# Kernel tuning notes

Measured on AMD Instinct MI355X. Metric: run time of the kernel, lower is better.

## Reference

```python
import jax, jax.numpy as jnp
import numpy as np

TEMPERATURE = 0.3
BASE_TEMPERATURE = 0.07
EPS = 1e-08


def setup_inputs() -> dict:
    key = jax.random.key(0)
    k1, k2 = jax.random.split(key)
    bsz, n_views, f_dim = 4096, 2, 128
    features = jax.random.normal(k1, (bsz, n_views, f_dim), dtype=jnp.float32)
    # L2-normalize as is standard for contrastive features (keeps logits well-scaled)
    features = features / jnp.linalg.norm(features, axis=-1, keepdims=True)
    labels = jax.random.randint(k2, (bsz,), 0, 2, dtype=jnp.int64)
    return {"features": features, "labels": labels}


def reference(features, labels):
    # features: [B, V, D], labels: [B]
    B, V, D = features.shape
    N = B * V

    # mask[i,j] = 1 if labels[i] == labels[j]
    mask = (labels[:, None] == labels[None, :]).astype(jnp.float32)  # [B, B]

    # torch.cat(torch.unbind(features, dim=1), dim=0): view-major stacking -> [V*B, D]
    contrast_feature = features.transpose(1, 0, 2).reshape(N, D)
    anchor_feature = contrast_feature  # contrast_mode == 'all'

    logits = jnp.matmul(anchor_feature, contrast_feature.T) / TEMPERATURE  # [N, N]
    logits = logits - jax.lax.stop_gradient(jnp.max(logits, axis=1, keepdims=True))

    mask = jnp.tile(mask, (V, V))  # [N, N]
    logits_mask = 1.0 - jnp.eye(N, dtype=jnp.float32)  # mask out self-contrast
    mask = mask * logits_mask

    exp_logits = jnp.exp(logits) * logits_mask
    log_prob = logits - jnp.log(jnp.sum(exp_logits, axis=1, keepdims=True) + EPS)

    mean_log_prob_pos = jnp.sum(mask * log_prob, axis=1) / (jnp.sum(mask, axis=1) + EPS)
    loss = -(TEMPERATURE / BASE_TEMPERATURE) * mean_log_prob_pos  # [N]
    return jnp.mean(loss.reshape(V, B))
```

## Files before the change

kernel.cpp:

```cpp
#include <hip/hip_runtime.h>
#include <hip/hip_bf16.h>

constexpr int B_SZ  = 4096;
constexpr int N_SZ  = 8192;
constexpr int CHUNK = 512;
constexpr int TILE  = 64;
constexpr int NT    = CHUNK / TILE;
constexpr int NCH   = N_SZ / CHUNK;
constexpr int BROWS = 128;

typedef __attribute__((ext_vector_type(8))) __bf16 bf16x8;
typedef __attribute__((ext_vector_type(4))) float f32x4;

#define SQRT_CSC  2.1929404f
#define SELF_EXP  28.0316248f
#define NEG_RATIO (-(0.3f / 0.07f))

__device__ __forceinline__ unsigned short f2bf(float f) {
    unsigned u = __float_as_uint(f);
    u += 0x7FFFu + ((u >> 16) & 1u);
    return (unsigned short)(u >> 16);
}

__device__ __forceinline__ void gl_lds16(const unsigned short* g, unsigned short* l) {
    __builtin_amdgcn_global_load_lds(
        (const __attribute__((address_space(1))) unsigned int*)g,
        (__attribute__((address_space(3))) unsigned int*)l, 16, 0, 0);
}

__global__ __launch_bounds__(256) void prep_kernel(const float* __restrict__ feat,
                                                   unsigned short* __restrict__ A,
                                                   float* __restrict__ out) {
    const int tid = threadIdx.x;
    if (blockIdx.x == 0 && tid == 0) out[0] = 0.f;
    int t = blockIdx.x * 256 + tid;
    int n = t >> 5;
    int q = (t & 31) << 2;
    int b = n & (B_SZ - 1);
    int v = n >> 12;
    const float4 f = *reinterpret_cast<const float4*>(feat + (((size_t)b * 2 + v) << 7) + q);
    ushort4 o;
    o.x = f2bf(f.x * SQRT_CSC); o.y = f2bf(f.y * SQRT_CSC);
    o.z = f2bf(f.z * SQRT_CSC); o.w = f2bf(f.w * SQRT_CSC);
    *reinterpret_cast<ushort4*>(A + (((size_t)n) << 7) + q) = o;
}

__global__ __launch_bounds__(256) void msum_kernel(const float* __restrict__ feat,
                                                   const int* __restrict__ labels,
                                                   float* __restrict__ mpart) {
    __shared__ float sm[2][256];
    const int tid = threadIdx.x;
    const int v = tid >> 7, d = tid & 127;
    const int b0 = blockIdx.x * 16;
    float a0 = 0.f, a1 = 0.f;
#pragma unroll
    for (int it = 0; it < 16; ++it) {
        const int b = b0 + it;
        const float x = feat[(((size_t)b * 2 + v) << 7) + d];
        if (labels[b]) a1 += x; else a0 += x;
    }
    sm[0][tid] = a0; sm[1][tid] = a1;
    __syncthreads();
    if (tid < 128)
        mpart[(size_t)tid * 256 + blockIdx.x] = sm[0][tid] + sm[0][tid + 128];
    else
        mpart[(size_t)tid * 256 + blockIdx.x] = sm[1][tid - 128] + sm[1][tid];
}

__global__ __launch_bounds__(256) void mreduce_kernel(const float* __restrict__ mpart,
                                                      const int* __restrict__ labels,
                                                      float* __restrict__ mvec,
                                                      int* __restrict__ cnt) {
    __shared__ int redi[4];
    const int tid = threadIdx.x;
    const float* p = mpart + (size_t)tid * 256;
    float s = 0.f;
#pragma unroll 8
    for (int k = 0; k < 256; k += 4) {
        const float4 x = *reinterpret_cast<const float4*>(p + k);
        s += x.x + x.y + x.z + x.w;
    }
    mvec[tid] = s;
    int c = 0;
    for (int i = tid; i < B_SZ; i += 256) c += labels[i];
#pragma unroll
    for (int m = 1; m < 64; m <<= 1) c += __shfl_xor(c, m);
    if ((tid & 63) == 0) redi[tid >> 6] = c;
    __syncthreads();
    if (tid == 0) *cnt = redi[0] + redi[1] + redi[2] + redi[3];
}

__global__ __launch_bounds__(256, 2) void gram_kernel(const unsigned short* __restrict__ A,
                                                      float* __restrict__ S_part) {
    __shared__ __align__(16) unsigned short tb[2][TILE * 128];

    const int tid  = threadIdx.x;
    const int wave = tid >> 6;
    const int lane = tid & 63;
    const int grp  = lane >> 4;
    const int lc   = lane & 15;
    const int row0 = blockIdx.x * BROWS + wave * 32;
    const int col0 = blockIdx.y * CHUNK;

    bf16x8 a[2][4];
#pragma unroll
    for (int rt = 0; rt < 2; ++rt) {
        const unsigned short* ap = A + ((size_t)(row0 + 16 * rt + lc) << 7) + grp * 8;
#pragma unroll
        for (int g = 0; g < 4; ++g)
            a[rt][g] = *reinterpret_cast<const bf16x8*>(ap + g * 32);
    }

    int off[4];
#pragma unroll
    for (int g = 0; g < 4; ++g)
        off[g] = lc * 128 + (((4 * g + grp) ^ (lc & 7)) << 3);

    float s_acc[2][4] = {{0,0,0,0},{0,0,0,0}};

    auto stage = [&](int buf, int tt) {
        const unsigned short* gbase = A + ((size_t)(col0 + tt * TILE) << 7);
#pragma unroll
        for (int k = 0; k < 4; ++k) {
            const int s = tid + 256 * k;
            const int r = s >> 4, c = s & 15;
            const int src = (r << 4) + (c ^ (r & 7));
            gl_lds16(gbase + src * 8, &tb[buf][s * 8]);
        }
    };

    stage(0, 0);
    __syncthreads();

#pragma clang loop unroll(disable)
    for (int t = 0; t < NT; ++t) {
        const int cur = t & 1;
        if (t + 1 < NT) stage(cur ^ 1, t + 1);

        const unsigned short* bp = &tb[cur][0];
#pragma unroll
        for (int ct = 0; ct < 4; ++ct) {
            bf16x8 bfr[4];
#pragma unroll
            for (int g = 0; g < 4; ++g)
                bfr[g] = *reinterpret_cast<const bf16x8*>(bp + ct * 2048 + off[g]);

            f32x4 acc0 = {0,0,0,0}, acc1 = {0,0,0,0};
#pragma unroll
            for (int g = 0; g < 4; ++g) {
                acc0 = __builtin_amdgcn_mfma_f32_16x16x32_bf16(a[0][g], bfr[g], acc0, 0, 0, 0);
                acc1 = __builtin_amdgcn_mfma_f32_16x16x32_bf16(a[1][g], bfr[g], acc1, 0, 0, 0);
            }
#pragma unroll
            for (int r = 0; r < 4; ++r) {
                s_acc[0][r] += __builtin_amdgcn_exp2f(acc0[r]);
                s_acc[1][r] += __builtin_amdgcn_exp2f(acc1[r]);
            }
        }
        __syncthreads();
    }

#pragma unroll
    for (int m = 1; m < 16; m <<= 1)
#pragma unroll
        for (int rt = 0; rt < 2; ++rt)
#pragma unroll
            for (int r = 0; r < 4; ++r)
                s_acc[rt][r] += __shfl_xor(s_acc[rt][r], m);

    if (lc == 0) {
        const size_t base = (size_t)blockIdx.y * N_SZ;
#pragma unroll
        for (int rt = 0; rt < 2; ++rt)
#pragma unroll
            for (int r = 0; r < 4; ++r)
                S_part[base + row0 + 16 * rt + 4 * grp + r] = s_acc[rt][r];
    }
}

__global__ __launch_bounds__(256) void final_kernel(const float* __restrict__ S_part,
                                                    const float* __restrict__ feat,
                                                    const int* __restrict__ labels,
                                                    const float* __restrict__ mvec,
                                                    const int* __restrict__ cnt,
                                                    float* __restrict__ out) {
    __shared__ float red[4];
    const int tid = threadIdx.x;
    const int i = blockIdx.x * 256 + tid;

    float S = -SELF_EXP;
#pragma unroll
    for (int k = 0; k < NCH; ++k) S += S_part[(size_t)k * N_SZ + i];

    const int b = i & (B_SZ - 1), v = i >> 12;
    const int lab = labels[b];
    const float* fr = feat + (((size_t)b * 2 + v) << 7);
    const float* mv = mvec + (lab ? 128 : 0);
    float dot = 0.f;
#pragma unroll 8
    for (int d = 0; d < 128; d += 4) {
        const float4 x = *reinterpret_cast<const float4*>(fr + d);
        const float4 y = *reinterpret_cast<const float4*>(mv + d);
        dot += x.x * y.x + x.y * y.y + x.z * y.z + x.w * y.w;
    }

    const int c1 = *cnt;
    const int cs = lab ? c1 : (B_SZ - c1);
    const float n = (float)(2 * cs - 1);
    float term = ((dot - 1.0f) * (1.0f / 0.3f) - n * logf(S + 1e-8f)) / (n + 1e-8f);

#pragma unroll
    for (int m = 1; m < 64; m <<= 1) term += __shfl_xor(term, m);
    if ((tid & 63) == 0) red[tid >> 6] = term;
    __syncthreads();
    if (tid == 0)
        atomicAdd(out, (red[0] + red[1] + red[2] + red[3]) * (NEG_RATIO / (float)N_SZ));
}

extern "C" void kernel_launch(void* const* d_in, const int* in_sizes, int n_in,
                              void* d_out, int out_size, void* d_ws, size_t ws_size,
                              hipStream_t stream) {
    const float* feat = (const float*)d_in[0];
    const int* labels = (const int*)d_in[1];
    float* out = (float*)d_out;

    char* ws = (char*)d_ws;
    unsigned short* A = (unsigned short*)ws;
    float* S_part = (float*)(ws + (size_t)2 * 1024 * 1024);
    float* mpart  = (float*)(ws + (size_t)2 * 1024 * 1024 + 512 * 1024);
    float* mvec   = (float*)(ws + (size_t)2 * 1024 * 1024 + 768 * 1024);
    int*   cnt    = (int*)(ws + (size_t)2 * 1024 * 1024 + 769 * 1024);

    prep_kernel<<<dim3(1024), dim3(256), 0, stream>>>(feat, A, out);
    msum_kernel<<<dim3(256), dim3(256), 0, stream>>>(feat, labels, mpart);
    mreduce_kernel<<<dim3(1), dim3(256), 0, stream>>>(mpart, labels, mvec, cnt);
    gram_kernel<<<dim3(N_SZ / BROWS, NCH), dim3(256), 0, stream>>>(A, S_part);
    final_kernel<<<dim3(N_SZ / 256), dim3(256), 0, stream>>>(S_part, feat, labels, mvec, cnt, out);
}
```

Measured before the change: 49.98 us.

## Exploit Gram matrix symmetry by computing only upper-triangular tiles

The Gram kernel now skips tiles below the diagonal and, for each computed tile, accumulates both row sums and column sums of exp(logits), so each off-diagonal product is reused for both rows. Diagonal-straddling tiles mask out self and lower entries, which removes the self-exp subtraction. The final kernel gathers row partials and column partials separately. This roughly halves the MFMA and exp work, at the cost of LDS atomics for column sums, extra partial-buffer traffic, and imbalance from early-exiting blocks.

```diff
diff --git a/kernel.cpp b/kernel.cpp
--- a/kernel.cpp
+++ b/kernel.cpp
@@ -3,17 +3,16 @@
 
 constexpr int B_SZ  = 4096;
 constexpr int N_SZ  = 8192;
-constexpr int CHUNK = 512;
+constexpr int CHUNK = 256;
 constexpr int TILE  = 64;
 constexpr int NT    = CHUNK / TILE;
-constexpr int NCH   = N_SZ / CHUNK;
-constexpr int BROWS = 128;
+constexpr int NRB   = N_SZ / 128;
+constexpr int NCB   = N_SZ / CHUNK;
 
 typedef __attribute__((ext_vector_type(8))) __bf16 bf16x8;
 typedef __attribute__((ext_vector_type(4))) float f32x4;
 
 #define SQRT_CSC  2.1929404f
-#define SELF_EXP  28.0316248f
 #define NEG_RATIO (-(0.3f / 0.07f))
 
 __device__ __forceinline__ unsigned short f2bf(float f) {
@@ -91,16 +90,24 @@
 }
 
 __global__ __launch_bounds__(256, 2) void gram_kernel(const unsigned short* __restrict__ A,
-                                                      float* __restrict__ S_part) {
+                                                      float* __restrict__ rowpart,
+                                                      float* __restrict__ colpart) {
+    const int bx = blockIdx.x, by = blockIdx.y;
+    if (by < (bx >> 1)) return;
+    const bool strad = (by == (bx >> 1));
+
     __shared__ __align__(16) unsigned short tb[2][TILE * 128];
+    __shared__ float colsum[CHUNK];
 
     const int tid  = threadIdx.x;
     const int wave = tid >> 6;
     const int lane = tid & 63;
     const int grp  = lane >> 4;
     const int lc   = lane & 15;
-    const int row0 = blockIdx.x * BROWS + wave * 32;
-    const int col0 = blockIdx.y * CHUNK;
+    const int row0 = bx * 128 + wave * 32;
+    const int col0 = by * CHUNK;
+
+    colsum[tid] = 0.f;
 
     bf16x8 a[2][4];
 #pragma unroll
@@ -151,11 +158,47 @@
                 acc0 = __builtin_amdgcn_mfma_f32_16x16x32_bf16(a[0][g], bfr[g], acc0, 0, 0, 0);
                 acc1 = __builtin_amdgcn_mfma_f32_16x16x32_bf16(a[1][g], bfr[g], acc1, 0, 0, 0);
             }
-#pragma unroll
-            for (int r = 0; r < 4; ++r) {
-                s_acc[0][r] += __builtin_amdgcn_exp2f(acc0[r]);
-                s_acc[1][r] += __builtin_amdgcn_exp2f(acc1[r]);
+
+            const int tcol = t * TILE + ct * 16 + lc;
+            float es0, es1;
+            if (strad) {
+                const int col = col0 + tcol;
+                float e00 = __builtin_amdgcn_exp2f(acc0[0]);
+                float e01 = __builtin_amdgcn_exp2f(acc0[1]);
+                float e02 = __builtin_amdgcn_exp2f(acc0[2]);
+                float e03 = __builtin_amdgcn_exp2f(acc0[3]);
+                float e10 = __builtin_amdgcn_exp2f(acc1[0]);
+                float e11 = __builtin_amdgcn_exp2f(acc1[1]);
+                float e12 = __builtin_amdgcn_exp2f(acc1[2]);
+                float e13 = __builtin_amdgcn_exp2f(acc1[3]);
+                const int r0 = row0 + 4 * grp;
+                e00 = (col > r0 + 0)      ? e00 : 0.f;
+                e01 = (col > r0 + 1)      ? e01 : 0.f;
+                e02 = (col > r0 + 2)      ? e02 : 0.f;
+                e03 = (col > r0 + 3)      ? e03 : 0.f;
+                e10 = (col > r0 + 16)     ? e10 : 0.f;
+                e11 = (col > r0 + 17)     ? e11 : 0.f;
+                e12 = (col > r0 + 18)     ? e12 : 0.f;
+                e13 = (col > r0 + 19)     ? e13 : 0.f;
+                s_acc[0][0] += e00; s_acc[0][1] += e01; s_acc[0][2] += e02; s_acc[0][3] += e03;
+                s_acc[1][0] += e10; s_acc[1][1] += e11; s_acc[1][2] += e12; s_acc[1][3] += e13;
+                es0 = (e00 + e01) + (e02 + e03);
+                es1 = (e10 + e11) + (e12 + e13);
+            } else {
+                float e00 = __builtin_amdgcn_exp2f(acc0[0]);
+                float e01 = __builtin_amdgcn_exp2f(acc0[1]);
+                float e02 = __builtin_amdgcn_exp2f(acc0[2]);
+                float e03 = __builtin_amdgcn_exp2f(acc0[3]);
+                float e10 = __builtin_amdgcn_exp2f(acc1[0]);
+                float e11 = __builtin_amdgcn_exp2f(acc1[1]);
+                float e12 = __builtin_amdgcn_exp2f(acc1[2]);
+                float e13 = __builtin_amdgcn_exp2f(acc1[3]);
+                s_acc[0][0] += e00; s_acc[0][1] += e01; s_acc[0][2] += e02; s_acc[0][3] += e03;
+                s_acc[1][0] += e10; s_acc[1][1] += e11; s_acc[1][2] += e12; s_acc[1][3] += e13;
+                es0 = (e00 + e01) + (e02 + e03);
+                es1 = (e10 + e11) + (e12 + e13);
             }
+            atomicAdd(&colsum[tcol], es0 + es1);
         }
         __syncthreads();
     }
@@ -169,16 +212,20 @@
                 s_acc[rt][r] += __shfl_xor(s_acc[rt][r], m);
 
     if (lc == 0) {
-        const size_t base = (size_t)blockIdx.y * N_SZ;
+        const size_t base = (size_t)by * N_SZ;
 #pragma unroll
         for (int rt = 0; rt < 2; ++rt)
 #pragma unroll
             for (int r = 0; r < 4; ++r)
-                S_part[base + row0 + 16 * rt + 4 * grp + r] = s_acc[rt][r];
-    }
-}
-
-__global__ __launch_bounds__(256) void final_kernel(const float* __restrict__ S_part,
+                rowpart[base + row0 + 16 * rt + 4 * grp + r] = s_acc[rt][r];
+    }
+
+    __syncthreads();
+    colpart[(size_t)bx * N_SZ + col0 + tid] = colsum[tid];
+}
+
+__global__ __launch_bounds__(256) void final_kernel(const float* __restrict__ rowpart,
+                                                    const float* __restrict__ colpart,
                                                     const float* __restrict__ feat,
                                                     const int* __restrict__ labels,
                                                     const float* __restrict__ mvec,
@@ -187,10 +234,12 @@
     __shared__ float red[4];
     const int tid = threadIdx.x;
     const int i = blockIdx.x * 256 + tid;
-
-    float S = -SELF_EXP;
-#pragma unroll
-    for (int k = 0; k < NCH; ++k) S += S_part[(size_t)k * N_SZ + i];
+    const int cb = i >> 8;
+
+    float S = 0.f;
+    for (int by = cb; by < NCB; ++by) S += rowpart[(size_t)by * N_SZ + i];
+    const int bxMax = 2 * cb + 1;
+    for (int bxx = 0; bxx <= bxMax; ++bxx) S += colpart[(size_t)bxx * N_SZ + i];
 
     const int b = i & (B_SZ - 1), v = i >> 12;
     const int lab = labels[b];
@@ -226,14 +275,15 @@
 
     char* ws = (char*)d_ws;
     unsigned short* A = (unsigned short*)ws;
-    float* S_part = (float*)(ws + (size_t)2 * 1024 * 1024);
-    float* mpart  = (float*)(ws + (size_t)2 * 1024 * 1024 + 512 * 1024);
-    float* mvec   = (float*)(ws + (size_t)2 * 1024 * 1024 + 768 * 1024);
-    int*   cnt    = (int*)(ws + (size_t)2 * 1024 * 1024 + 769 * 1024);
+    float* rowpart = (float*)(ws + (size_t)2 * 1024 * 1024);
+    float* colpart = (float*)(ws + (size_t)3 * 1024 * 1024);
+    float* mpart   = (float*)(ws + (size_t)5 * 1024 * 1024);
+    float* mvec    = (float*)(ws + (size_t)5 * 1024 * 1024 + 256 * 1024);
+    int*   cnt     = (int*)(ws + (size_t)5 * 1024 * 1024 + 257 * 1024);
 
     prep_kernel<<<dim3(1024), dim3(256), 0, stream>>>(feat, A, out);
     msum_kernel<<<dim3(256), dim3(256), 0, stream>>>(feat, labels, mpart);
     mreduce_kernel<<<dim3(1), dim3(256), 0, stream>>>(mpart, labels, mvec, cnt);
-    gram_kernel<<<dim3(N_SZ / BROWS, NCH), dim3(256), 0, stream>>>(A, S_part);
-    final_kernel<<<dim3(N_SZ / 256), dim3(256), 0, stream>>>(S_part, feat, labels, mvec, cnt, out);
-}
+    gram_kernel<<<dim3(NRB, NCB), dim3(256), 0, stream>>>(A, rowpart, colpart);
+    final_kernel<<<dim3(N_SZ / 256), dim3(256), 0, stream>>>(rowpart, colpart, feat, labels, mvec, cnt, out);
+}
```

After: 92.15 us. 1.84x slower.
